# Optimization experiments

Measured on AMD Instinct MI355X. Metric: run time of the kernel, lower is better.

Reference implementation:

```python
import jax, jax.numpy as jnp
import numpy as np

B, N, M, H = 16, 2048, 512, 512


def setup_inputs() -> dict:
    key = jax.random.key(0)
    ks = jax.random.split(key, 14)
    s = 0.02  # weight init scale
    return {
        "A": jax.random.uniform(ks[0], (B, N, N), dtype=jnp.float32),
        "h": jax.random.normal(ks[1], (B, N, M), dtype=jnp.float32),
        # fcv: Linear(m,H) -> ReLU -> Linear(H,H); weights stored [in,out]
        "Wv1": jax.random.normal(ks[2], (M, H), dtype=jnp.float32) * s,
        "bv1": jnp.zeros((H,), jnp.float32),
        "Wv2": jax.random.normal(ks[3], (H, H), dtype=jnp.float32) * s,
        "bv2": jnp.zeros((H,), jnp.float32),
        "Wk": jax.random.normal(ks[4], (M, H), dtype=jnp.float32) * s,
        "bk": jnp.zeros((H,), jnp.float32),
        "Wq": jax.random.normal(ks[5], (M, H), dtype=jnp.float32) * s,
        "bq": jnp.zeros((H,), jnp.float32),
        "Wout": jax.random.normal(ks[6], (H, M), dtype=jnp.float32) * s,
        "bout": jnp.zeros((M,), jnp.float32),
    }


def reference(A, h, Wv1, bv1, Wv2, bv2, Wk, bk, Wq, bq, Wout, bout):
    # v = relu(fcv(h)) where fcv = Lin -> ReLU -> Lin
    v = jax.nn.relu(jax.nn.relu(h @ Wv1 + bv1) @ Wv2 + bv2)      # [B,N,H]
    q = jax.nn.relu(h @ Wq + bq)                                  # [B,N,H]
    k = jax.nn.relu(h @ Wk + bk)                                  # [B,N,H]
    # att = softmax((q @ k^T) * -A, axis=2)
    scores = jnp.einsum("bnh,bmh->bnm", q, k) * -A                # [B,N,N]
    att = jax.nn.softmax(scores, axis=2)
    out = jnp.einsum("bnm,bmh->bnh", att, v) + v                  # [B,N,H]
    return jax.nn.relu(out @ Wout + bout)                         # [B,N,M]
```

## Files before the change

kernel.cpp:

```cpp
#include <hip/hip_runtime.h>

typedef __bf16 bf16;
typedef bf16 bf16x4 __attribute__((ext_vector_type(4)));
typedef bf16 bf16x8 __attribute__((ext_vector_type(8)));
typedef float f32x4 __attribute__((ext_vector_type(4)));

static constexpr int BATCH = 16;
static constexpr int SEQ   = 2048;
static constexpr int DH    = 512;
static constexpr int ROWS  = BATCH * SEQ;

__device__ __forceinline__ f32x4 mfma16(bf16x8 a, bf16x8 b, f32x4 c) {
    return __builtin_amdgcn_mfma_f32_16x16x32_bf16(a, b, c, 0, 0, 0);
}

__device__ __forceinline__ void gl_lds16(const void* g, void* l) {
    __builtin_amdgcn_global_load_lds((const __attribute__((address_space(1))) void*)g,
                                     (__attribute__((address_space(3))) void*)l, 16, 0, 0);
}

__global__ void cvt_bf16_kernel(const float* __restrict__ in, bf16* __restrict__ out, int n4) {
    int i = blockIdx.x * blockDim.x + threadIdx.x;
    const int stride = gridDim.x * blockDim.x;
    for (; i < n4; i += stride) {
        f32x4 f = *reinterpret_cast<const f32x4*>(in + (size_t)i * 4);
        bf16x4 o;
        o[0] = (bf16)f[0]; o[1] = (bf16)f[1]; o[2] = (bf16)f[2]; o[3] = (bf16)f[3];
        *reinterpret_cast<bf16x4*>(out + (size_t)i * 4) = o;
    }
}

__global__ void cvt_wT5_kernel(const float* __restrict__ w0, const float* __restrict__ w1,
                               const float* __restrict__ w2, const float* __restrict__ w3,
                               const float* __restrict__ w4, bf16* __restrict__ out) {
    const int t = blockIdx.y;
    const float* in = (t == 0) ? w0 : (t == 1) ? w1 : (t == 2) ? w2 : (t == 3) ? w3 : w4;
    int idx = blockIdx.x * 256 + threadIdx.x;
    int n = idx >> 9, k = idx & 511;
    out[t * 262144 + idx] = (bf16)in[k * 512 + n];
}

template <int OMODE>
__global__ __launch_bounds__(256, 2)
void gemm_relu_kernel(const bf16* __restrict__ X, const bf16* __restrict__ Wt,
                      const float* __restrict__ bias,
                      bf16* __restrict__ Y, bf16* __restrict__ Yt,
                      float* __restrict__ Yf)
{
    __shared__ bf16 Xl[2][128 * 64];
    __shared__ bf16 Wl[2][128 * 64];

    const int tid = threadIdx.x;
    const int lane = tid & 63, wid = tid >> 6;
    const int wr = wid >> 1, wc = wid & 1;
    const int id = blockIdx.x;
    const int r0 = (((id >> 5) << 3) + (id & 7)) * 128;
    const int c0 = ((id >> 3) & 3) * 128;
    const int lrow = lane & 15, lhi = lane >> 4;

    const int srow = tid >> 3;
    const int skb  = (tid & 7) ^ (srow & 7);
    const int sdst = wid * 512;

    auto stage = [&](int buf, int kc) {
        const bf16* xs = X + (size_t)r0 * 512 + kc * 64;
        const bf16* ws = Wt + (size_t)c0 * 512 + kc * 64;
        #pragma unroll
        for (int c = 0; c < 4; ++c) {
            const int row = c * 32 + srow;
            gl_lds16(xs + (size_t)row * 512 + skb * 8, &Xl[buf][c * 2048 + sdst]);
        }
        #pragma unroll
        for (int c = 0; c < 4; ++c) {
            const int row = c * 32 + srow;
            gl_lds16(ws + (size_t)row * 512 + skb * 8, &Wl[buf][c * 2048 + sdst]);
        }
    };

    f32x4 acc[4][4] = {};

    stage(0, 0);

    for (int t = 0; t < 8; ++t) {
        const int buf = t & 1;
        if (t + 1 < 8) {
            stage(buf ^ 1, t + 1);
            asm volatile("s_waitcnt vmcnt(8)" ::: "memory");
        } else {
            asm volatile("s_waitcnt vmcnt(0)" ::: "memory");
        }
        __builtin_amdgcn_s_barrier();
        __builtin_amdgcn_sched_barrier(0);

        #pragma unroll
        for (int kk = 0; kk < 2; ++kk) {
            bf16x8 af[4], bfr[4];
            const int kb = kk * 4 + lhi;
            #pragma unroll
            for (int tt = 0; tt < 4; ++tt) {
                const int ra = wr * 64 + tt * 16 + lrow;
                af[tt] = *reinterpret_cast<const bf16x8*>(&Xl[buf][ra * 64 + ((kb ^ (ra & 7)) * 8)]);
            }
            #pragma unroll
            for (int tt = 0; tt < 4; ++tt) {
                const int rb = wc * 64 + tt * 16 + lrow;
                bfr[tt] = *reinterpret_cast<const bf16x8*>(&Wl[buf][rb * 64 + ((kb ^ (rb & 7)) * 8)]);
            }
            #pragma unroll
            for (int i = 0; i < 4; ++i)
                #pragma unroll
                for (int j = 0; j < 4; ++j)
                    acc[i][j] = mfma16(af[i], bfr[j], acc[i][j]);
        }

        asm volatile("s_waitcnt lgkmcnt(0)" ::: "memory");
        __builtin_amdgcn_s_barrier();
        __builtin_amdgcn_sched_barrier(0);
    }

    #pragma unroll
    for (int i = 0; i < 4; ++i) {
        #pragma unroll
        for (int j = 0; j < 4; ++j) {
            const int col = c0 + wc * 64 + j * 16 + lrow;
            const float bb = bias[col];
            #pragma unroll
            for (int rg = 0; rg < 4; ++rg) {
                const int r = r0 + wr * 64 + i * 16 + lhi * 4 + rg;
                float y = acc[i][j][rg] + bb;
                y = y > 0.f ? y : 0.f;
                if (OMODE == 2) {
                    Yf[(size_t)r * 512 + col] = y;
                } else {
                    Y[(size_t)r * 512 + col] = (bf16)y;
                    if (OMODE == 1) {
                        const int bi = r >> 11, nn = r & 2047;
                        Yt[((size_t)bi * 512 + col) * 2048 + nn] = (bf16)y;
                    }
                }
            }
        }
    }
}

__global__ __launch_bounds__(512, 1)
void attn_kernel(const bf16* __restrict__ Q, const bf16* __restrict__ K,
                 const bf16* __restrict__ Vt, const bf16* __restrict__ V,
                 const float* __restrict__ A, bf16* __restrict__ O)
{
    __shared__ bf16 K_lds[128 * 512];
    __shared__ bf16 P_lds[64 * 144];
    __shared__ float sump_lds[2][64];

    const int tid = threadIdx.x;
    const int lane = tid & 63, wid = tid >> 6;
    const int wr = wid >> 1, wc = wid & 1;
    const int lrow = lane & 15, lhi = lane >> 4;

    const int id = blockIdx.x;
    const int xcd = id & 7, j = id >> 3;
    const int bb = 2 * xcd + (j >> 5);
    const int n0 = (j & 31) * 64;
    const int srow_base = wr * 16 + lhi * 4;

    const bf16* Kbase  = K + (size_t)bb * SEQ * DH;
    const bf16* Vtbase = Vt + (size_t)bb * DH * SEQ;

    #pragma unroll
    for (int c = 0; c < 16; ++c) {
        const int row = wid * 16 + c;
        gl_lds16(Kbase + (size_t)row * DH + ((lane ^ (row & 7)) * 8), &K_lds[row * 512]);
    }

    bf16x8 qf[16];
    {
        const bf16* qp = Q + (size_t)(bb * SEQ + n0 + wr * 16 + lrow) * DH + lhi * 8;
        #pragma unroll
        for (int kk = 0; kk < 16; ++kk)
            qf[kk] = *reinterpret_cast<const bf16x8*>(qp + kk * 32);
    }

    float l_part[4] = {};
    f32x4 acc[4][4] = {};

    __syncthreads();

    for (int it = 0; it < 16; ++it) {
        const int m0 = it * 128;

        float av[16];
        {
            const float* ap = A + ((size_t)bb * SEQ + n0 + srow_base) * SEQ + m0 + wc * 64 + lrow;
            #pragma unroll
            for (int sc = 0; sc < 4; ++sc)
                #pragma unroll
                for (int rg = 0; rg < 4; ++rg)
                    av[sc * 4 + rg] = ap[(size_t)rg * SEQ + sc * 16];
        }

        f32x4 s[4] = {};
        {
            #pragma unroll
            for (int kk = 0; kk < 16; ++kk) {
                const int ks = kk * 4 + lhi;
                #pragma unroll
                for (int sc = 0; sc < 4; ++sc) {
                    const int kr = wc * 64 + sc * 16 + lrow;
                    bf16x8 kf = *reinterpret_cast<const bf16x8*>(
                        &K_lds[kr * 512 + ((ks ^ (kr & 7)) * 8)]);
                    s[sc] = mfma16(qf[kk], kf, s[sc]);
                }
            }
        }

        #pragma unroll
        for (int sc = 0; sc < 4; ++sc) {
            #pragma unroll
            for (int rg = 0; rg < 4; ++rg) {
                const float p = __expf(s[sc][rg] * (-av[sc * 4 + rg]));
                const int row = srow_base + rg;
                P_lds[row * 144 + wc * 64 + sc * 16 + lrow] = (bf16)p;
                l_part[rg] += p;
            }
        }

        asm volatile("s_waitcnt lgkmcnt(0)" ::: "memory");
        __builtin_amdgcn_s_barrier();
        __builtin_amdgcn_sched_barrier(0);

        if (it + 1 < 16) {
            #pragma unroll
            for (int c = 0; c < 16; ++c) {
                const int row = wid * 16 + c;
                gl_lds16(Kbase + (size_t)(m0 + 128 + row) * DH + ((lane ^ (row & 7)) * 8),
                         &K_lds[row * 512]);
            }
        }

        {
            const bf16* vp = Vtbase + (size_t)(wid * 64 + lrow) * SEQ + m0 + lhi * 8;
            bf16x8 vfk[2][4];
            #pragma unroll
            for (int ht = 0; ht < 4; ++ht)
                vfk[0][ht] = *reinterpret_cast<const bf16x8*>(vp + (size_t)(ht * 16) * SEQ);
            #pragma unroll
            for (int kc = 0; kc < 4; ++kc) {
                if (kc + 1 < 4) {
                    #pragma unroll
                    for (int ht = 0; ht < 4; ++ht)
                        vfk[(kc + 1) & 1][ht] = *reinterpret_cast<const bf16x8*>(
                            vp + (size_t)(ht * 16) * SEQ + (kc + 1) * 32);
                }
                #pragma unroll
                for (int t = 0; t < 4; ++t) {
                    const bf16x8 pf = *reinterpret_cast<const bf16x8*>(
                        &P_lds[(t * 16 + lrow) * 144 + kc * 32 + lhi * 8]);
                    #pragma unroll
                    for (int ht = 0; ht < 4; ++ht)
                        acc[t][ht] = mfma16(pf, vfk[kc & 1][ht], acc[t][ht]);
                }
            }
        }

        asm volatile("s_waitcnt lgkmcnt(0)" ::: "memory");
        __builtin_amdgcn_s_barrier();
        __builtin_amdgcn_sched_barrier(0);
    }

    #pragma unroll
    for (int rg = 0; rg < 4; ++rg) {
        float sv = l_part[rg];
        sv += __shfl_xor(sv, 1);
        sv += __shfl_xor(sv, 2);
        sv += __shfl_xor(sv, 4);
        sv += __shfl_xor(sv, 8);
        if (lrow == 0) sump_lds[wc][srow_base + rg] = sv;
    }
    __syncthreads();

    #pragma unroll
    for (int t = 0; t < 4; ++t) {
        #pragma unroll
        for (int rg = 0; rg < 4; ++rg) {
            const int row = t * 16 + lhi * 4 + rg;
            const float inv = 1.f / (sump_lds[0][row] + sump_lds[1][row]);
            const size_t rbase = (size_t)(bb * SEQ + n0 + row) * DH;
            #pragma unroll
            for (int ht = 0; ht < 4; ++ht) {
                const int col = wid * 64 + ht * 16 + lrow;
                const float vv = (float)V[rbase + col];
                O[rbase + col] = (bf16)(acc[t][ht][rg] * inv + vv);
            }
        }
    }
}

extern "C" void kernel_launch(void* const* d_in, const int* in_sizes, int n_in,
                              void* d_out, int out_size, void* d_ws, size_t ws_size,
                              hipStream_t stream) {
    const float* A    = (const float*)d_in[0];
    const float* h    = (const float*)d_in[1];
    const float* Wv1  = (const float*)d_in[2];
    const float* bv1  = (const float*)d_in[3];
    const float* Wv2  = (const float*)d_in[4];
    const float* bv2  = (const float*)d_in[5];
    const float* Wk   = (const float*)d_in[6];
    const float* bk   = (const float*)d_in[7];
    const float* Wq   = (const float*)d_in[8];
    const float* bq   = (const float*)d_in[9];
    const float* Wout = (const float*)d_in[10];
    const float* bout = (const float*)d_in[11];
    float* out = (float*)d_out;

    char* ws = (char*)d_ws;
    const size_t SZ = (size_t)ROWS * 512 * sizeof(bf16);
    bf16* hb   = (bf16*)(ws + 0 * SZ);
    bf16* tq   = (bf16*)(ws + 1 * SZ);
    bf16* kb   = (bf16*)(ws + 2 * SZ);
    bf16* vb   = (bf16*)(ws + 3 * SZ);
    bf16* vtb  = (bf16*)(ws + 4 * SZ);
    bf16* wbase = (bf16*)(ws + 5 * SZ);
    bf16* Wv1t  = wbase + 0 * 262144;
    bf16* Wv2t  = wbase + 1 * 262144;
    bf16* Wqt   = wbase + 2 * 262144;
    bf16* Wkt   = wbase + 3 * 262144;
    bf16* Woutt = wbase + 4 * 262144;
    bf16* ob = hb;

    cvt_bf16_kernel<<<4096, 256, 0, stream>>>(h, hb, ROWS * 512 / 4);
    cvt_wT5_kernel<<<dim3(1024, 5), 256, 0, stream>>>(Wv1, Wv2, Wq, Wk, Wout, wbase);

    gemm_relu_kernel<0><<<1024, 256, 0, stream>>>(hb, Wv1t, bv1, tq, nullptr, nullptr);
    gemm_relu_kernel<1><<<1024, 256, 0, stream>>>(tq, Wv2t, bv2, vb, vtb, nullptr);
    gemm_relu_kernel<0><<<1024, 256, 0, stream>>>(hb, Wqt, bq, tq, nullptr, nullptr);
    gemm_relu_kernel<0><<<1024, 256, 0, stream>>>(hb, Wkt, bk, kb, nullptr, nullptr);

    attn_kernel<<<dim3(512), 512, 0, stream>>>(tq, kb, vtb, vb, A, ob);

    gemm_relu_kernel<2><<<1024, 256, 0, stream>>>(ob, Woutt, bout, nullptr, nullptr, out);
}
```

Measured before the change: 479.9 us.

## Merge conversion kernels, XOR-swizzle P tile in LDS, add MFMA priority hints

Fuses the h bf16 conversion and the weight transpose-conversion into one launch, removing one kernel launch and its tail. In the attention kernel, the padded P buffer (stride 144) becomes an unpadded stride-128 layout with an XOR swizzle on 8-element blocks, which saves LDS and is meant to avoid bank conflicts on both the write and the bf16x8 reads. It also wraps the QK and PV MFMA loops in s_setprio to favour matrix issue over the other waves. The swizzle makes the indexing more complex, and the priority hints may have little effect at one block per CU.

```diff
diff --git a/kernel.cpp b/kernel.cpp
--- a/kernel.cpp
+++ b/kernel.cpp
@@ -19,25 +19,30 @@
                                      (__attribute__((address_space(3))) void*)l, 16, 0, 0);
 }
 
-__global__ void cvt_bf16_kernel(const float* __restrict__ in, bf16* __restrict__ out, int n4) {
-    int i = blockIdx.x * blockDim.x + threadIdx.x;
-    const int stride = gridDim.x * blockDim.x;
-    for (; i < n4; i += stride) {
-        f32x4 f = *reinterpret_cast<const f32x4*>(in + (size_t)i * 4);
-        bf16x4 o;
-        o[0] = (bf16)f[0]; o[1] = (bf16)f[1]; o[2] = (bf16)f[2]; o[3] = (bf16)f[3];
-        *reinterpret_cast<bf16x4*>(out + (size_t)i * 4) = o;
-    }
-}
-
-__global__ void cvt_wT5_kernel(const float* __restrict__ w0, const float* __restrict__ w1,
+__global__ void cvt_all_kernel(const float* __restrict__ h,
+                               const float* __restrict__ w0, const float* __restrict__ w1,
                                const float* __restrict__ w2, const float* __restrict__ w3,
-                               const float* __restrict__ w4, bf16* __restrict__ out) {
-    const int t = blockIdx.y;
-    const float* in = (t == 0) ? w0 : (t == 1) ? w1 : (t == 2) ? w2 : (t == 3) ? w3 : w4;
-    int idx = blockIdx.x * 256 + threadIdx.x;
-    int n = idx >> 9, k = idx & 511;
-    out[t * 262144 + idx] = (bf16)in[k * 512 + n];
+                               const float* __restrict__ w4,
+                               bf16* __restrict__ hb, bf16* __restrict__ wout) {
+    const int b = blockIdx.x;
+    if (b < 4096) {
+        const int n4 = ROWS * 512 / 4;
+        int i = b * 256 + threadIdx.x;
+        const int stride = 4096 * 256;
+        for (; i < n4; i += stride) {
+            f32x4 f = *reinterpret_cast<const f32x4*>(h + (size_t)i * 4);
+            bf16x4 o;
+            o[0] = (bf16)f[0]; o[1] = (bf16)f[1]; o[2] = (bf16)f[2]; o[3] = (bf16)f[3];
+            *reinterpret_cast<bf16x4*>(hb + (size_t)i * 4) = o;
+        }
+    } else {
+        const int bb = b - 4096;
+        const int t = bb >> 10;
+        const float* in = (t == 0) ? w0 : (t == 1) ? w1 : (t == 2) ? w2 : (t == 3) ? w3 : w4;
+        int idx = (bb & 1023) * 256 + threadIdx.x;
+        int n = idx >> 9, k = idx & 511;
+        wout[t * 262144 + idx] = (bf16)in[k * 512 + n];
+    }
 }
 
 template <int OMODE>
@@ -149,7 +154,7 @@
                  const float* __restrict__ A, bf16* __restrict__ O)
 {
     __shared__ bf16 K_lds[128 * 512];
-    __shared__ bf16 P_lds[64 * 144];
+    __shared__ bf16 P_lds[64 * 128];
     __shared__ float sump_lds[2][64];
 
     const int tid = threadIdx.x;
@@ -200,6 +205,7 @@
 
         f32x4 s[4] = {};
         {
+            __builtin_amdgcn_s_setprio(1);
             #pragma unroll
             for (int kk = 0; kk < 16; ++kk) {
                 const int ks = kk * 4 + lhi;
@@ -211,6 +217,7 @@
                     s[sc] = mfma16(qf[kk], kf, s[sc]);
                 }
             }
+            __builtin_amdgcn_s_setprio(0);
         }
 
         #pragma unroll
@@ -219,7 +226,8 @@
             for (int rg = 0; rg < 4; ++rg) {
                 const float p = __expf(s[sc][rg] * (-av[sc * 4 + rg]));
                 const int row = srow_base + rg;
-                P_lds[row * 144 + wc * 64 + sc * 16 + lrow] = (bf16)p;
+                const int blk = wc * 8 + sc * 2 + (lrow >> 3);
+                P_lds[row * 128 + ((blk ^ (row & 7)) * 8) + (lrow & 7)] = (bf16)p;
                 l_part[rg] += p;
             }
         }
@@ -251,14 +259,17 @@
                         vfk[(kc + 1) & 1][ht] = *reinterpret_cast<const bf16x8*>(
                             vp + (size_t)(ht * 16) * SEQ + (kc + 1) * 32);
                 }
+                __builtin_amdgcn_s_setprio(1);
                 #pragma unroll
                 for (int t = 0; t < 4; ++t) {
+                    const int prow = t * 16 + lrow;
                     const bf16x8 pf = *reinterpret_cast<const bf16x8*>(
-                        &P_lds[(t * 16 + lrow) * 144 + kc * 32 + lhi * 8]);
+                        &P_lds[prow * 128 + (((kc * 4 + lhi) ^ (prow & 7)) * 8)]);
                     #pragma unroll
                     for (int ht = 0; ht < 4; ++ht)
                         acc[t][ht] = mfma16(pf, vfk[kc & 1][ht], acc[t][ht]);
                 }
+                __builtin_amdgcn_s_setprio(0);
             }
         }
 
@@ -327,8 +338,7 @@
     bf16* Woutt = wbase + 4 * 262144;
     bf16* ob = hb;
 
-    cvt_bf16_kernel<<<4096, 256, 0, stream>>>(h, hb, ROWS * 512 / 4);
-    cvt_wT5_kernel<<<dim3(1024, 5), 256, 0, stream>>>(Wv1, Wv2, Wq, Wk, Wout, wbase);
+    cvt_all_kernel<<<9216, 256, 0, stream>>>(h, Wv1, Wv2, Wq, Wk, Wout, hb, wbase);
 
     gemm_relu_kernel<0><<<1024, 256, 0, stream>>>(hb, Wv1t, bv1, tq, nullptr, nullptr);
     gemm_relu_kernel<1><<<1024, 256, 0, stream>>>(tq, Wv2t, bv2, vb, vtb, nullptr);
```

Result: faster. 450.1 us (-6.2%).
